# Kernel optimization log

Hardware: AMD Instinct MI355X
Metric: run time of the kernel (lower is better)

## Reference

```python
import jax, jax.numpy as jnp
import numpy as np

INPUT, HIDDEN = 2048, 128

def setup_inputs() -> dict:
    key = jax.random.key(0)
    ks = jax.random.split(key, 8)
    B, T = 64, 512
    s_ih = 1.0 / np.sqrt(HIDDEN)  # pytorch RNN init: U(-1/sqrt(H), 1/sqrt(H))
    x = jax.random.normal(ks[0], (B, T, INPUT), dtype=jnp.float32)
    W_ih = jax.random.uniform(ks[1], (HIDDEN, INPUT), jnp.float32, -s_ih, s_ih)
    W_hh = jax.random.uniform(ks[2], (HIDDEN, HIDDEN), jnp.float32, -s_ih, s_ih)
    b_ih = jax.random.uniform(ks[3], (HIDDEN,), jnp.float32, -s_ih, s_ih)
    b_hh = jax.random.uniform(ks[4], (HIDDEN,), jnp.float32, -s_ih, s_ih)
    W_fc = jax.random.uniform(ks[5], (1, HIDDEN), jnp.float32, -s_ih, s_ih)
    b_fc = jax.random.uniform(ks[6], (1,), jnp.float32, -s_ih, s_ih)
    return {"x": x, "W_ih": W_ih, "W_hh": W_hh, "b_ih": b_ih, "b_hh": b_hh,
            "W_fc": W_fc, "b_fc": b_fc}

def reference(x, W_ih, W_hh, b_ih, b_hh, W_fc, b_fc):
    B = x.shape[0]
    # Batched input projection for all timesteps: [B, T, H]
    xw = jnp.einsum('bti,hi->bth', x, W_ih) + b_ih + b_hh
    # Sequential hidden-to-hidden recurrence: h_t = tanh(xw_t + h_{t-1} @ W_hh^T)
    def step(h, xw_t):
        h_new = jnp.tanh(xw_t + h @ W_hh.T)
        return h_new, None
    h0 = jnp.zeros((B, HIDDEN), dtype=x.dtype)
    h_last, _ = jax.lax.scan(step, h0, jnp.swapaxes(xw, 0, 1))  # scan over time
    # dropout is identity in eval mode
    logits = h_last @ W_fc.T + b_fc  # [B, 1]
    return logits
```

## Files before the change

kernel.cpp:

```cpp
#include <hip/hip_runtime.h>
#include <hip/hip_bf16.h>
#include <math.h>

#define INPUT 2048
#define HIDDEN 128
#define BATCH 64
#define TSTEPS 512
#define RB 16

typedef _Float16 half_t;
typedef __attribute__((ext_vector_type(2))) _Float16 half2_t;
typedef __attribute__((ext_vector_type(8))) _Float16 f16x8;
typedef __attribute__((ext_vector_type(4))) float f32x4;

static __device__ __forceinline__ f16x8 as_f16x8(uint4 v) {
  return __builtin_bit_cast(f16x8, v);
}
static __device__ __forceinline__ unsigned int h2u(half2_t v) {
  return __builtin_bit_cast(unsigned int, v);
}
static __device__ __forceinline__ half2_t pkrtz(float a, float b) {
  return __builtin_bit_cast(half2_t, __builtin_amdgcn_cvt_pkrtz(a, b));
}
static __device__ __forceinline__ float h2f(unsigned short u) {
  return (float)__builtin_bit_cast(half_t, u);
}

static __device__ __forceinline__ float tanh_fast(float x) {
#if __has_builtin(__builtin_amdgcn_exp2f)
  const float e = __builtin_amdgcn_exp2f(x * 2.885390082f);
#else
  const float e = exp2f(x * 2.885390082f);
#endif
  return 1.f - 2.f * __builtin_amdgcn_rcpf(e + 1.f);
}

__global__ __launch_bounds__(256) void prep_kernel(
    const float* __restrict__ W_ih, const float* __restrict__ W_hh,
    uint4* __restrict__ Wg, unsigned int* __restrict__ Whh2) {
  const int id = blockIdx.x * 256 + threadIdx.x;
  const int col = id & 127;
  const int kc = id >> 7;
  const float4 a = *(const float4*)(W_ih + (size_t)col * INPUT + kc * 8);
  const float4 b = *(const float4*)(W_ih + (size_t)col * INPUT + kc * 8 + 4);
  uint4 q = {h2u(pkrtz(a.x, a.y)), h2u(pkrtz(a.z, a.w)),
             h2u(pkrtz(b.x, b.y)), h2u(pkrtz(b.z, b.w))};
  Wg[(size_t)kc * 128 + col] = q;
  if (id < 8192) {
    float2 p = ((const float2*)W_hh)[id];
    half_t ha = (half_t)p.x, hb = (half_t)p.y;
    Whh2[id] = (unsigned int)__builtin_bit_cast(unsigned short, ha) |
               ((unsigned int)__builtin_bit_cast(unsigned short, hb) << 16);
  }
}

#define GBM 64
#define GBK 64
#define GNKT (INPUT / GBK)

__global__ __launch_bounds__(256) void gemm_xw_f16(
    const float* __restrict__ x, const uint4* __restrict__ Wg,
    const float* __restrict__ b_ih, const float* __restrict__ b_hh,
    half_t* __restrict__ xw) {
  __shared__ uint4 sA[2][8][64];

  const int tid = threadIdx.x;
  const int lane = tid & 63;
  const int w = tid >> 6;
  const int wr = w >> 1, wc = w & 1;
  const int block_row = blockIdx.x * GBM;
  const int kcl = lane >> 4;
  const int l15 = lane & 15;

  const int xm = tid & 63, xkq = tid >> 6;
  const float* xsrc = x + (size_t)(block_row + xm) * INPUT + xkq * 16;

  f32x4 acc[2][4];
#pragma unroll
  for (int rt = 0; rt < 2; ++rt)
#pragma unroll
    for (int ct = 0; ct < 4; ++ct) acc[rt][ct] = (f32x4)0.f;

  float bias_c[4];
#pragma unroll
  for (int ct = 0; ct < 4; ++ct) {
    const int col = wc * 64 + ct * 16 + l15;
    bias_c[ct] = b_ih[col] + b_hh[col];
  }

  float4 xva[4], xvb[4];
  uint4 br0[8], br1[8];

  auto XLOAD = [&](int kt, float4* xv) {
    const float4* xs = (const float4*)(xsrc + kt * GBK);
#pragma unroll
    for (int j = 0; j < 4; ++j) xv[j] = xs[j];
  };
  auto XWRITE = [&](int bf, const float4* xv) {
#pragma unroll
    for (int g = 0; g < 2; ++g) {
      uint4 q = {h2u(pkrtz(xv[2 * g].x, xv[2 * g].y)),
                 h2u(pkrtz(xv[2 * g].z, xv[2 * g].w)),
                 h2u(pkrtz(xv[2 * g + 1].x, xv[2 * g + 1].y)),
                 h2u(pkrtz(xv[2 * g + 1].z, xv[2 * g + 1].w))};
      sA[bf][xkq * 2 + g][xm] = q;
    }
  };
  auto BLOAD = [&](int kt, uint4* bb) {
#pragma unroll
    for (int kf = 0; kf < 2; ++kf)
#pragma unroll
      for (int ct = 0; ct < 4; ++ct)
        bb[kf * 4 + ct] =
            Wg[(size_t)(kt * 8 + kf * 4 + kcl) * 128 + wc * 64 + ct * 16 + l15];
  };
  auto COMPUTE = [&](int bf, const uint4* bb) {
    uint4 af[2][2];
#pragma unroll
    for (int kf = 0; kf < 2; ++kf)
#pragma unroll
      for (int rt = 0; rt < 2; ++rt)
        af[kf][rt] = sA[bf][kf * 4 + kcl][wr * 32 + rt * 16 + l15];
#pragma unroll
    for (int kf = 0; kf < 2; ++kf)
#pragma unroll
      for (int rt = 0; rt < 2; ++rt)
#pragma unroll
        for (int ct = 0; ct < 4; ++ct)
          acc[rt][ct] = __builtin_amdgcn_mfma_f32_16x16x32_f16(
              as_f16x8(af[kf][rt]), as_f16x8(bb[kf * 4 + ct]), acc[rt][ct], 0, 0, 0);
  };

  XLOAD(0, xva);
  XLOAD(1, xvb);
  BLOAD(0, br0);
  XWRITE(0, xva);
  __syncthreads();

#pragma unroll 1
  for (int kt = 0; kt < GNKT; kt += 2) {
    BLOAD(kt + 1, br1);
    if (kt + 2 < GNKT) XLOAD(kt + 2, xva);
    COMPUTE(0, br0);
    XWRITE(1, xvb);
    __syncthreads();
    if (kt + 2 < GNKT) BLOAD(kt + 2, br0);
    if (kt + 3 < GNKT) XLOAD(kt + 3, xvb);
    COMPUTE(1, br1);
    if (kt + 2 < GNKT) {
      XWRITE(0, xva);
      __syncthreads();
    }
  }

  const int rbase = block_row + wr * 32 + (lane >> 4) * 4;
#pragma unroll
  for (int rt = 0; rt < 2; ++rt)
#pragma unroll
    for (int ct = 0; ct < 4; ++ct) {
      const int col = wc * 64 + ct * 16 + l15;
#pragma unroll
      for (int j = 0; j < 4; ++j) {
        const int row = rbase + rt * 16 + j;
        xw[(size_t)row * HIDDEN + col] = (half_t)(acc[rt][ct][j] + bias_c[ct]);
      }
    }
}

__global__ __launch_bounds__(256) void rnn_rec_mfma(
    const half_t* __restrict__ xw, const unsigned int* __restrict__ Whh2,
    const float* __restrict__ W_fc, const float* __restrict__ b_fc,
    float* __restrict__ out) {
  const int blk = blockIdx.x;
  const int tid = threadIdx.x;
  const int lane = tid & 63;
  const int w = tid >> 6;
  const int bl = lane & 15;
  const int g = lane >> 4;
  const int swz = (bl & 7) << 4;

  __shared__ half_t st[2][RB][HIDDEN];
  __shared__ float red[256];

  uint4 afr[2][4];
#pragma unroll
  for (int mi = 0; mi < 2; ++mi)
#pragma unroll
    for (int kt = 0; kt < 4; ++kt)
      afr[mi][kt] = *(const uint4*)(Whh2 + ((size_t)((2 * w + mi) * 16 + bl)) * 64 +
                                    kt * 16 + g * 4);

#pragma unroll
  for (int i = 0; i < 4; ++i) ((unsigned int*)st)[tid + 256 * i] = 0u;
  __syncthreads();

  const half_t* xb0 = xw + ((size_t)(blk * RB + bl) * TSTEPS) * HIDDEN + w * 32 + g * 4;
  const half_t* xb1 = xb0 + 16;

  float hh[2][4];

  auto STEP = [&](const half_t* stR, half_t* stW, ushort4 xc0, ushort4 xc1) {
    uint4 bfr[4];
#pragma unroll
    for (int kt = 0; kt < 4; ++kt) {
      const int off = (bl * 256 + kt * 64 + g * 16) ^ swz;
      bfr[kt] = *(const uint4*)((const char*)stR + off);
    }
    f32x4 a0, a1;
    a0[0] = h2f(xc0.x); a0[1] = h2f(xc0.y); a0[2] = h2f(xc0.z); a0[3] = h2f(xc0.w);
    a1[0] = h2f(xc1.x); a1[1] = h2f(xc1.y); a1[2] = h2f(xc1.z); a1[3] = h2f(xc1.w);
#pragma unroll
    for (int kt = 0; kt < 4; ++kt) {
      a0 = __builtin_amdgcn_mfma_f32_16x16x32_f16(as_f16x8(afr[0][kt]),
                                                  as_f16x8(bfr[kt]), a0, 0, 0, 0);
      a1 = __builtin_amdgcn_mfma_f32_16x16x32_f16(as_f16x8(afr[1][kt]),
                                                  as_f16x8(bfr[kt]), a1, 0, 0, 0);
    }
#pragma unroll
    for (int j = 0; j < 4; ++j) {
      hh[0][j] = tanh_fast(a0[j]);
      hh[1][j] = tanh_fast(a1[j]);
    }
    uint2 p0 = {h2u(pkrtz(hh[0][0], hh[0][1])), h2u(pkrtz(hh[0][2], hh[0][3]))};
    uint2 p1 = {h2u(pkrtz(hh[1][0], hh[1][1])), h2u(pkrtz(hh[1][2], hh[1][3]))};
    const int w0 = (bl * 256 + (2 * w + 0) * 32 + g * 8) ^ swz;
    const int w1 = (bl * 256 + (2 * w + 1) * 32 + g * 8) ^ swz;
    *(uint2*)((char*)stW + w0) = p0;
    *(uint2*)((char*)stW + w1) = p1;
    __syncthreads();
  };

  ushort4 xA0 = *(const ushort4*)(xb0);
  ushort4 xA1 = *(const ushort4*)(xb1);
  ushort4 xB0 = *(const ushort4*)(xb0 + HIDDEN);
  ushort4 xB1 = *(const ushort4*)(xb1 + HIDDEN);

  for (int t2 = 0; t2 < TSTEPS; t2 += 2) {
    ushort4 c0 = xA0, c1 = xA1;
    xA0 = *(const ushort4*)(xb0 + (size_t)(t2 + 2) * HIDDEN);
    xA1 = *(const ushort4*)(xb1 + (size_t)(t2 + 2) * HIDDEN);
    STEP(&st[0][0][0], &st[1][0][0], c0, c1);

    ushort4 d0 = xB0, d1 = xB1;
    xB0 = *(const ushort4*)(xb0 + (size_t)(t2 + 3) * HIDDEN);
    xB1 = *(const ushort4*)(xb1 + (size_t)(t2 + 3) * HIDDEN);
    STEP(&st[1][0][0], &st[0][0][0], d0, d1);
  }

  const float4 wf0 = *(const float4*)&W_fc[(2 * w + 0) * 16 + g * 4];
  const float4 wf1 = *(const float4*)&W_fc[(2 * w + 1) * 16 + g * 4];
  float partial = hh[0][0] * wf0.x + hh[0][1] * wf0.y + hh[0][2] * wf0.z +
                  hh[0][3] * wf0.w + hh[1][0] * wf1.x + hh[1][1] * wf1.y +
                  hh[1][2] * wf1.z + hh[1][3] * wf1.w;
  red[tid] = partial;
  __syncthreads();
  if (tid < RB) {
    float s = b_fc[0];
#pragma unroll
    for (int q = 0; q < 16; ++q) s += red[q * 16 + tid];
    out[blk * RB + tid] = s;
  }
}

extern "C" void kernel_launch(void* const* d_in, const int* in_sizes, int n_in,
                              void* d_out, int out_size, void* d_ws, size_t ws_size,
                              hipStream_t stream) {
  const float* x    = (const float*)d_in[0];
  const float* W_ih = (const float*)d_in[1];
  const float* W_hh = (const float*)d_in[2];
  const float* b_ih = (const float*)d_in[3];
  const float* b_hh = (const float*)d_in[4];
  const float* W_fc = (const float*)d_in[5];
  const float* b_fc = (const float*)d_in[6];

  char* ws = (char*)d_ws;
  half_t*       xwf16 = (half_t*)ws;
  uint4*        Wg    = (uint4*)(ws + (8u << 20));
  unsigned int* Whh2  = (unsigned int*)(ws + (8u << 20) + (512u << 10));

  prep_kernel<<<128, 256, 0, stream>>>(W_ih, W_hh, Wg, Whh2);
  gemm_xw_f16<<<(BATCH * TSTEPS) / GBM, 256, 0, stream>>>(x, Wg, b_ih, b_hh, xwf16);
  rnn_rec_mfma<<<BATCH / RB, 256, 0, stream>>>(xwf16, Whh2, W_fc, b_fc, (float*)d_out);
}
```

Measured before the change: 259.2 us.

## Process two 16-row batch tiles per block in the recurrence kernel

The recurrence kernel now handles 32 batch rows per block (two 16-row MFMA tiles sharing the same W_hh fragments), launching 2 blocks instead of 4. Each step issues twice as many independent MFMAs and LDS reads between barriers, so the per-step barrier and latency costs are amortised over more work. The trade-off is less parallelism across CUs and a longer dependent chain per step. The final reduction is extended to produce both tiles' outputs.

```diff
diff --git a/kernel.cpp b/kernel.cpp
--- a/kernel.cpp
+++ b/kernel.cpp
@@ -167,7 +167,7 @@
     }
 }
 
-__global__ __launch_bounds__(256) void rnn_rec_mfma(
+__global__ __launch_bounds__(256, 1) void rnn_rec_mfma2(
     const half_t* __restrict__ xw, const unsigned int* __restrict__ Whh2,
     const float* __restrict__ W_fc, const float* __restrict__ b_fc,
     float* __restrict__ out) {
@@ -176,11 +176,11 @@
   const int lane = tid & 63;
   const int w = tid >> 6;
   const int bl = lane & 15;
-  const int g = lane >> 4;
+  const int kg = lane >> 4;
   const int swz = (bl & 7) << 4;
 
-  __shared__ half_t st[2][RB][HIDDEN];
-  __shared__ float red[256];
+  __shared__ half_t st[2][2][RB][HIDDEN];
+  __shared__ float red[512];
 
   uint4 afr[2][4];
 #pragma unroll
@@ -188,77 +188,122 @@
 #pragma unroll
     for (int kt = 0; kt < 4; ++kt)
       afr[mi][kt] = *(const uint4*)(Whh2 + ((size_t)((2 * w + mi) * 16 + bl)) * 64 +
-                                    kt * 16 + g * 4);
-
-#pragma unroll
-  for (int i = 0; i < 4; ++i) ((unsigned int*)st)[tid + 256 * i] = 0u;
+                                    kt * 16 + kg * 4);
+
+#pragma unroll
+  for (int i = 0; i < 8; ++i) ((unsigned int*)st)[tid + 256 * i] = 0u;
   __syncthreads();
 
-  const half_t* xb0 = xw + ((size_t)(blk * RB + bl) * TSTEPS) * HIDDEN + w * 32 + g * 4;
-  const half_t* xb1 = xb0 + 16;
-
-  float hh[2][4];
-
-  auto STEP = [&](const half_t* stR, half_t* stW, ushort4 xc0, ushort4 xc1) {
-    uint4 bfr[4];
+  const half_t* p00 = xw + ((size_t)(blk * 32 + bl) * TSTEPS) * HIDDEN + w * 32 + kg * 4;
+  const half_t* p01 = p00 + 16;
+  const half_t* p10 = xw + ((size_t)(blk * 32 + 16 + bl) * TSTEPS) * HIDDEN + w * 32 + kg * 4;
+  const half_t* p11 = p10 + 16;
+
+  float hh[2][2][4];
+
+  int roff0[4], roff1[4];
+#pragma unroll
+  for (int kt = 0; kt < 4; ++kt) {
+    roff0[kt] = ((bl * 256 + kt * 64 + kg * 16) ^ swz);
+    roff1[kt] = roff0[kt] + 4096;
+  }
+  const int w00 = ((bl * 256 + (2 * w + 0) * 32 + kg * 8) ^ swz);
+  const int w01 = ((bl * 256 + (2 * w + 1) * 32 + kg * 8) ^ swz);
+  const int w10 = w00 + 4096, w11 = w01 + 4096;
+
+  auto STEP2 = [&](const char* stR, char* stW, ushort4 c00, ushort4 c01,
+                   ushort4 c10, ushort4 c11) {
+    uint4 b0[4], b1[4];
+#pragma unroll
+    for (int kt = 0; kt < 4; ++kt) b0[kt] = *(const uint4*)(stR + roff0[kt]);
+#pragma unroll
+    for (int kt = 0; kt < 4; ++kt) b1[kt] = *(const uint4*)(stR + roff1[kt]);
+
+    f32x4 a00, a01, a10, a11;
+    a00[0] = h2f(c00.x); a00[1] = h2f(c00.y); a00[2] = h2f(c00.z); a00[3] = h2f(c00.w);
+    a01[0] = h2f(c01.x); a01[1] = h2f(c01.y); a01[2] = h2f(c01.z); a01[3] = h2f(c01.w);
+    a10[0] = h2f(c10.x); a10[1] = h2f(c10.y); a10[2] = h2f(c10.z); a10[3] = h2f(c10.w);
+    a11[0] = h2f(c11.x); a11[1] = h2f(c11.y); a11[2] = h2f(c11.z); a11[3] = h2f(c11.w);
+
 #pragma unroll
     for (int kt = 0; kt < 4; ++kt) {
-      const int off = (bl * 256 + kt * 64 + g * 16) ^ swz;
-      bfr[kt] = *(const uint4*)((const char*)stR + off);
-    }
-    f32x4 a0, a1;
-    a0[0] = h2f(xc0.x); a0[1] = h2f(xc0.y); a0[2] = h2f(xc0.z); a0[3] = h2f(xc0.w);
-    a1[0] = h2f(xc1.x); a1[1] = h2f(xc1.y); a1[2] = h2f(xc1.z); a1[3] = h2f(xc1.w);
-#pragma unroll
-    for (int kt = 0; kt < 4; ++kt) {
-      a0 = __builtin_amdgcn_mfma_f32_16x16x32_f16(as_f16x8(afr[0][kt]),
-                                                  as_f16x8(bfr[kt]), a0, 0, 0, 0);
-      a1 = __builtin_amdgcn_mfma_f32_16x16x32_f16(as_f16x8(afr[1][kt]),
-                                                  as_f16x8(bfr[kt]), a1, 0, 0, 0);
+      a00 = __builtin_amdgcn_mfma_f32_16x16x32_f16(as_f16x8(afr[0][kt]),
+                                                   as_f16x8(b0[kt]), a00, 0, 0, 0);
+      a01 = __builtin_amdgcn_mfma_f32_16x16x32_f16(as_f16x8(afr[1][kt]),
+                                                   as_f16x8(b0[kt]), a01, 0, 0, 0);
+      a10 = __builtin_amdgcn_mfma_f32_16x16x32_f16(as_f16x8(afr[0][kt]),
+                                                   as_f16x8(b1[kt]), a10, 0, 0, 0);
+      a11 = __builtin_amdgcn_mfma_f32_16x16x32_f16(as_f16x8(afr[1][kt]),
+                                                   as_f16x8(b1[kt]), a11, 0, 0, 0);
     }
 #pragma unroll
     for (int j = 0; j < 4; ++j) {
-      hh[0][j] = tanh_fast(a0[j]);
-      hh[1][j] = tanh_fast(a1[j]);
-    }
-    uint2 p0 = {h2u(pkrtz(hh[0][0], hh[0][1])), h2u(pkrtz(hh[0][2], hh[0][3]))};
-    uint2 p1 = {h2u(pkrtz(hh[1][0], hh[1][1])), h2u(pkrtz(hh[1][2], hh[1][3]))};
-    const int w0 = (bl * 256 + (2 * w + 0) * 32 + g * 8) ^ swz;
-    const int w1 = (bl * 256 + (2 * w + 1) * 32 + g * 8) ^ swz;
-    *(uint2*)((char*)stW + w0) = p0;
-    *(uint2*)((char*)stW + w1) = p1;
+      hh[0][0][j] = tanh_fast(a00[j]);
+      hh[0][1][j] = tanh_fast(a01[j]);
+      hh[1][0][j] = tanh_fast(a10[j]);
+      hh[1][1][j] = tanh_fast(a11[j]);
+    }
+    uint2 q00 = {h2u(pkrtz(hh[0][0][0], hh[0][0][1])), h2u(pkrtz(hh[0][0][2], hh[0][0][3]))};
+    uint2 q01 = {h2u(pkrtz(hh[0][1][0], hh[0][1][1])), h2u(pkrtz(hh[0][1][2], hh[0][1][3]))};
+    uint2 q10 = {h2u(pkrtz(hh[1][0][0], hh[1][0][1])), h2u(pkrtz(hh[1][0][2], hh[1][0][3]))};
+    uint2 q11 = {h2u(pkrtz(hh[1][1][0], hh[1][1][1])), h2u(pkrtz(hh[1][1][2], hh[1][1][3]))};
+    *(uint2*)(stW + w00) = q00;
+    *(uint2*)(stW + w01) = q01;
+    *(uint2*)(stW + w10) = q10;
+    *(uint2*)(stW + w11) = q11;
     __syncthreads();
   };
 
-  ushort4 xA0 = *(const ushort4*)(xb0);
-  ushort4 xA1 = *(const ushort4*)(xb1);
-  ushort4 xB0 = *(const ushort4*)(xb0 + HIDDEN);
-  ushort4 xB1 = *(const ushort4*)(xb1 + HIDDEN);
+  char* st0 = (char*)&st[0][0][0][0];
+  char* st1 = (char*)&st[1][0][0][0];
+
+  ushort4 xa00 = *(const ushort4*)(p00);
+  ushort4 xa01 = *(const ushort4*)(p01);
+  ushort4 xa10 = *(const ushort4*)(p10);
+  ushort4 xa11 = *(const ushort4*)(p11);
+  ushort4 xb00 = *(const ushort4*)(p00 + HIDDEN);
+  ushort4 xb01 = *(const ushort4*)(p01 + HIDDEN);
+  ushort4 xb10 = *(const ushort4*)(p10 + HIDDEN);
+  ushort4 xb11 = *(const ushort4*)(p11 + HIDDEN);
 
   for (int t2 = 0; t2 < TSTEPS; t2 += 2) {
-    ushort4 c0 = xA0, c1 = xA1;
-    xA0 = *(const ushort4*)(xb0 + (size_t)(t2 + 2) * HIDDEN);
-    xA1 = *(const ushort4*)(xb1 + (size_t)(t2 + 2) * HIDDEN);
-    STEP(&st[0][0][0], &st[1][0][0], c0, c1);
-
-    ushort4 d0 = xB0, d1 = xB1;
-    xB0 = *(const ushort4*)(xb0 + (size_t)(t2 + 3) * HIDDEN);
-    xB1 = *(const ushort4*)(xb1 + (size_t)(t2 + 3) * HIDDEN);
-    STEP(&st[1][0][0], &st[0][0][0], d0, d1);
-  }
-
-  const float4 wf0 = *(const float4*)&W_fc[(2 * w + 0) * 16 + g * 4];
-  const float4 wf1 = *(const float4*)&W_fc[(2 * w + 1) * 16 + g * 4];
-  float partial = hh[0][0] * wf0.x + hh[0][1] * wf0.y + hh[0][2] * wf0.z +
-                  hh[0][3] * wf0.w + hh[1][0] * wf1.x + hh[1][1] * wf1.y +
-                  hh[1][2] * wf1.z + hh[1][3] * wf1.w;
-  red[tid] = partial;
+    const ushort4 c00 = xa00, c01 = xa01, c10 = xa10, c11 = xa11;
+    xa00 = *(const ushort4*)(p00 + (size_t)(t2 + 2) * HIDDEN);
+    xa01 = *(const ushort4*)(p01 + (size_t)(t2 + 2) * HIDDEN);
+    xa10 = *(const ushort4*)(p10 + (size_t)(t2 + 2) * HIDDEN);
+    xa11 = *(const ushort4*)(p11 + (size_t)(t2 + 2) * HIDDEN);
+    STEP2(st0, st1, c00, c01, c10, c11);
+
+    const ushort4 d00 = xb00, d01 = xb01, d10 = xb10, d11 = xb11;
+    xb00 = *(const ushort4*)(p00 + (size_t)(t2 + 3) * HIDDEN);
+    xb01 = *(const ushort4*)(p01 + (size_t)(t2 + 3) * HIDDEN);
+    xb10 = *(const ushort4*)(p10 + (size_t)(t2 + 3) * HIDDEN);
+    xb11 = *(const ushort4*)(p11 + (size_t)(t2 + 3) * HIDDEN);
+    STEP2(st1, st0, d00, d01, d10, d11);
+  }
+
+  const float4 wf0 = *(const float4*)&W_fc[(2 * w + 0) * 16 + kg * 4];
+  const float4 wf1 = *(const float4*)&W_fc[(2 * w + 1) * 16 + kg * 4];
+  float part0 = hh[0][0][0] * wf0.x + hh[0][0][1] * wf0.y + hh[0][0][2] * wf0.z +
+                hh[0][0][3] * wf0.w + hh[0][1][0] * wf1.x + hh[0][1][1] * wf1.y +
+                hh[0][1][2] * wf1.z + hh[0][1][3] * wf1.w;
+  float part1 = hh[1][0][0] * wf0.x + hh[1][0][1] * wf0.y + hh[1][0][2] * wf0.z +
+                hh[1][0][3] * wf0.w + hh[1][1][0] * wf1.x + hh[1][1][1] * wf1.y +
+                hh[1][1][2] * wf1.z + hh[1][1][3] * wf1.w;
+  red[tid] = part0;
+  red[256 + tid] = part1;
   __syncthreads();
   if (tid < RB) {
     float s = b_fc[0];
 #pragma unroll
     for (int q = 0; q < 16; ++q) s += red[q * 16 + tid];
-    out[blk * RB + tid] = s;
+    out[blk * 32 + tid] = s;
+  } else if (tid < 32) {
+    const int b2 = tid - 16;
+    float s = b_fc[0];
+#pragma unroll
+    for (int q = 0; q < 16; ++q) s += red[256 + q * 16 + b2];
+    out[blk * 32 + 16 + b2] = s;
   }
 }
 
@@ -280,5 +325,5 @@
 
   prep_kernel<<<128, 256, 0, stream>>>(W_ih, W_hh, Wg, Whh2);
   gemm_xw_f16<<<(BATCH * TSTEPS) / GBM, 256, 0, stream>>>(x, Wg, b_ih, b_hh, xwf16);
-  rnn_rec_mfma<<<BATCH / RB, 256, 0, stream>>>(xwf16, Whh2, W_fc, b_fc, (float*)d_out);
-}
+  rnn_rec_mfma2<<<2, 256, 0, stream>>>(xwf16, Whh2, W_fc, b_fc, (float*)d_out);
+}
```

Result: slower. 403.7 us (+55.7%).

## Fuse input GEMM and recurrence into one persistent kernel with per-timestep flags

Applied to the files above, without the earlier changes.

Merges the input-projection GEMM and the sequential recurrence into one launch. Four blocks run the recurrence while the rest compute xw per timestep, split-K into four slices that accumulate in order through atomic flags. The recurrence spins on each timestep's flag, so it can start before the whole GEMM finishes and overlap with it. The xw layout becomes time-major, and a large LDS pad limits blocks per CU, likely so the recurrence blocks get their own CUs. Risks are spin-wait and flag overhead, serialized split-K read-modify-writes, reduced GEMM occupancy, and reliance on the scheduler placing the recurrence blocks early.

```diff
diff --git a/kernel.cpp b/kernel.cpp
--- a/kernel.cpp
+++ b/kernel.cpp
@@ -7,6 +7,10 @@
 #define BATCH 64
 #define TSTEPS 512
 #define RB 16
+#define KSLICE 4
+#define KS (INPUT / KSLICE)
+#define GBK 64
+#define SNKT (KS / GBK)
 
 typedef _Float16 half_t;
 typedef __attribute__((ext_vector_type(2))) _Float16 half2_t;
@@ -54,133 +58,148 @@
   }
 }
 
-#define GBM 64
-#define GBK 64
-#define GNKT (INPUT / GBK)
-
-__global__ __launch_bounds__(256) void gemm_xw_f16(
+__global__ __launch_bounds__(256) void fused_kernel(
     const float* __restrict__ x, const uint4* __restrict__ Wg,
-    const float* __restrict__ b_ih, const float* __restrict__ b_hh,
-    half_t* __restrict__ xw) {
+    const unsigned int* __restrict__ Whh2, const float* __restrict__ b_ih,
+    const float* __restrict__ b_hh, const float* __restrict__ W_fc,
+    const float* __restrict__ b_fc, half_t* __restrict__ xw,
+    int* __restrict__ flags, float* __restrict__ out) {
   __shared__ uint4 sA[2][8][64];
+  __shared__ half_t st[2][RB][HIDDEN];
+  __shared__ float red[256];
+  __shared__ char lds_pad[39 * 1024];
+  if (flags == nullptr) lds_pad[threadIdx.x] = 1;
 
   const int tid = threadIdx.x;
   const int lane = tid & 63;
   const int w = tid >> 6;
-  const int wr = w >> 1, wc = w & 1;
-  const int block_row = blockIdx.x * GBM;
-  const int kcl = lane >> 4;
   const int l15 = lane & 15;
 
-  const int xm = tid & 63, xkq = tid >> 6;
-  const float* xsrc = x + (size_t)(block_row + xm) * INPUT + xkq * 16;
-
-  f32x4 acc[2][4];
-#pragma unroll
-  for (int rt = 0; rt < 2; ++rt)
-#pragma unroll
-    for (int ct = 0; ct < 4; ++ct) acc[rt][ct] = (f32x4)0.f;
-
-  float bias_c[4];
-#pragma unroll
-  for (int ct = 0; ct < 4; ++ct) {
-    const int col = wc * 64 + ct * 16 + l15;
-    bias_c[ct] = b_ih[col] + b_hh[col];
-  }
-
-  float4 xva[4], xvb[4];
-  uint4 br0[8], br1[8];
-
-  auto XLOAD = [&](int kt, float4* xv) {
-    const float4* xs = (const float4*)(xsrc + kt * GBK);
-#pragma unroll
-    for (int j = 0; j < 4; ++j) xv[j] = xs[j];
-  };
-  auto XWRITE = [&](int bf, const float4* xv) {
-#pragma unroll
-    for (int g = 0; g < 2; ++g) {
-      uint4 q = {h2u(pkrtz(xv[2 * g].x, xv[2 * g].y)),
-                 h2u(pkrtz(xv[2 * g].z, xv[2 * g].w)),
-                 h2u(pkrtz(xv[2 * g + 1].x, xv[2 * g + 1].y)),
-                 h2u(pkrtz(xv[2 * g + 1].z, xv[2 * g + 1].w))};
-      sA[bf][xkq * 2 + g][xm] = q;
-    }
-  };
-  auto BLOAD = [&](int kt, uint4* bb) {
-#pragma unroll
-    for (int kf = 0; kf < 2; ++kf)
-#pragma unroll
-      for (int ct = 0; ct < 4; ++ct)
-        bb[kf * 4 + ct] =
-            Wg[(size_t)(kt * 8 + kf * 4 + kcl) * 128 + wc * 64 + ct * 16 + l15];
-  };
-  auto COMPUTE = [&](int bf, const uint4* bb) {
-    uint4 af[2][2];
-#pragma unroll
-    for (int kf = 0; kf < 2; ++kf)
-#pragma unroll
-      for (int rt = 0; rt < 2; ++rt)
-        af[kf][rt] = sA[bf][kf * 4 + kcl][wr * 32 + rt * 16 + l15];
-#pragma unroll
-    for (int kf = 0; kf < 2; ++kf)
-#pragma unroll
-      for (int rt = 0; rt < 2; ++rt)
-#pragma unroll
-        for (int ct = 0; ct < 4; ++ct)
-          acc[rt][ct] = __builtin_amdgcn_mfma_f32_16x16x32_f16(
-              as_f16x8(af[kf][rt]), as_f16x8(bb[kf * 4 + ct]), acc[rt][ct], 0, 0, 0);
-  };
-
-  XLOAD(0, xva);
-  XLOAD(1, xvb);
-  BLOAD(0, br0);
-  XWRITE(0, xva);
-  __syncthreads();
-
-#pragma unroll 1
-  for (int kt = 0; kt < GNKT; kt += 2) {
-    BLOAD(kt + 1, br1);
-    if (kt + 2 < GNKT) XLOAD(kt + 2, xva);
-    COMPUTE(0, br0);
-    XWRITE(1, xvb);
-    __syncthreads();
-    if (kt + 2 < GNKT) BLOAD(kt + 2, br0);
-    if (kt + 3 < GNKT) XLOAD(kt + 3, xvb);
-    COMPUTE(1, br1);
-    if (kt + 2 < GNKT) {
-      XWRITE(0, xva);
-      __syncthreads();
-    }
-  }
-
-  const int rbase = block_row + wr * 32 + (lane >> 4) * 4;
-#pragma unroll
-  for (int rt = 0; rt < 2; ++rt)
+  if (blockIdx.x >= 4) {
+    const int p = blockIdx.x - 4;
+    const int t = p >> 2;
+    const int s = p & 3;
+
+    const int wr = w >> 1, wc = w & 1;
+    const int kcl = lane >> 4;
+    const int xm = tid & 63, xkq = tid >> 6;
+    const float* xsrc =
+        x + ((size_t)xm * TSTEPS + t) * INPUT + s * KS + xkq * 16;
+
+    f32x4 acc[2][4];
+#pragma unroll
+    for (int rt = 0; rt < 2; ++rt)
+#pragma unroll
+      for (int ct = 0; ct < 4; ++ct) acc[rt][ct] = (f32x4)0.f;
+
+    float bias_c[4];
 #pragma unroll
     for (int ct = 0; ct < 4; ++ct) {
       const int col = wc * 64 + ct * 16 + l15;
-#pragma unroll
-      for (int j = 0; j < 4; ++j) {
-        const int row = rbase + rt * 16 + j;
-        xw[(size_t)row * HIDDEN + col] = (half_t)(acc[rt][ct][j] + bias_c[ct]);
+      bias_c[ct] = b_ih[col] + b_hh[col];
+    }
+
+    float4 xva[4], xvb[4];
+    uint4 br0[8], br1[8];
+
+    auto XLOAD = [&](int kt, float4* xv) {
+      const float4* xs = (const float4*)(xsrc + kt * GBK);
+#pragma unroll
+      for (int j = 0; j < 4; ++j) xv[j] = xs[j];
+    };
+    auto XWRITE = [&](int bf, const float4* xv) {
+#pragma unroll
+      for (int g = 0; g < 2; ++g) {
+        uint4 q = {h2u(pkrtz(xv[2 * g].x, xv[2 * g].y)),
+                   h2u(pkrtz(xv[2 * g].z, xv[2 * g].w)),
+                   h2u(pkrtz(xv[2 * g + 1].x, xv[2 * g + 1].y)),
+                   h2u(pkrtz(xv[2 * g + 1].z, xv[2 * g + 1].w))};
+        sA[bf][xkq * 2 + g][xm] = q;
       }
-    }
-}
-
-__global__ __launch_bounds__(256) void rnn_rec_mfma(
-    const half_t* __restrict__ xw, const unsigned int* __restrict__ Whh2,
-    const float* __restrict__ W_fc, const float* __restrict__ b_fc,
-    float* __restrict__ out) {
+    };
+    auto BLOAD = [&](int kt, uint4* bb) {
+#pragma unroll
+      for (int kf = 0; kf < 2; ++kf)
+#pragma unroll
+        for (int ct = 0; ct < 4; ++ct)
+          bb[kf * 4 + ct] = Wg[(size_t)((s * SNKT + kt) * 8 + kf * 4 + kcl) * 128 +
+                               wc * 64 + ct * 16 + l15];
+    };
+    auto COMPUTE = [&](int bf, const uint4* bb) {
+      uint4 af[2][2];
+#pragma unroll
+      for (int kf = 0; kf < 2; ++kf)
+#pragma unroll
+        for (int rt = 0; rt < 2; ++rt)
+          af[kf][rt] = sA[bf][kf * 4 + kcl][wr * 32 + rt * 16 + l15];
+#pragma unroll
+      for (int kf = 0; kf < 2; ++kf)
+#pragma unroll
+        for (int rt = 0; rt < 2; ++rt)
+#pragma unroll
+          for (int ct = 0; ct < 4; ++ct)
+            acc[rt][ct] = __builtin_amdgcn_mfma_f32_16x16x32_f16(
+                as_f16x8(af[kf][rt]), as_f16x8(bb[kf * 4 + ct]), acc[rt][ct], 0, 0, 0);
+    };
+
+    XLOAD(0, xva);
+    XLOAD(1, xvb);
+    BLOAD(0, br0);
+    XWRITE(0, xva);
+    __syncthreads();
+
+#pragma unroll 1
+    for (int kt = 0; kt < SNKT; kt += 2) {
+      BLOAD(kt + 1, br1);
+      if (kt + 2 < SNKT) XLOAD(kt + 2, xva);
+      COMPUTE(0, br0);
+      XWRITE(1, xvb);
+      __syncthreads();
+      if (kt + 2 < SNKT) BLOAD(kt + 2, br0);
+      if (kt + 3 < SNKT) XLOAD(kt + 3, xvb);
+      COMPUTE(1, br1);
+      if (kt + 2 < SNKT) {
+        XWRITE(0, xva);
+        __syncthreads();
+      }
+    }
+
+    if (s != 0) {
+      if (tid == 0)
+        while (__hip_atomic_load(&flags[t], __ATOMIC_ACQUIRE,
+                                 __HIP_MEMORY_SCOPE_AGENT) != s)
+          __builtin_amdgcn_s_sleep(1);
+      __syncthreads();
+    }
+    const int rbase = wr * 32 + (lane >> 4) * 4;
+    half_t* xwt = xw + (size_t)t * (BATCH * HIDDEN);
+#pragma unroll
+    for (int rt = 0; rt < 2; ++rt)
+#pragma unroll
+      for (int ct = 0; ct < 4; ++ct) {
+        const int col = wc * 64 + ct * 16 + l15;
+#pragma unroll
+        for (int j = 0; j < 4; ++j) {
+          const int row = rbase + rt * 16 + j;
+          const size_t idx = (size_t)row * HIDDEN + col;
+          if (s == 0) {
+            xwt[idx] = (half_t)(acc[rt][ct][j] + bias_c[ct]);
+          } else {
+            xwt[idx] = (half_t)((float)xwt[idx] + acc[rt][ct][j]);
+          }
+        }
+      }
+    __syncthreads();
+    if (tid == 0)
+      __hip_atomic_store(&flags[t], s + 1, __ATOMIC_RELEASE,
+                         __HIP_MEMORY_SCOPE_AGENT);
+    return;
+  }
+
   const int blk = blockIdx.x;
-  const int tid = threadIdx.x;
-  const int lane = tid & 63;
-  const int w = tid >> 6;
   const int bl = lane & 15;
-  const int g = lane >> 4;
+  const int kg = lane >> 4;
   const int swz = (bl & 7) << 4;
-
-  __shared__ half_t st[2][RB][HIDDEN];
-  __shared__ float red[256];
 
   uint4 afr[2][4];
 #pragma unroll
@@ -188,22 +207,31 @@
 #pragma unroll
     for (int kt = 0; kt < 4; ++kt)
       afr[mi][kt] = *(const uint4*)(Whh2 + ((size_t)((2 * w + mi) * 16 + bl)) * 64 +
-                                    kt * 16 + g * 4);
+                                    kt * 16 + kg * 4);
 
 #pragma unroll
   for (int i = 0; i < 4; ++i) ((unsigned int*)st)[tid + 256 * i] = 0u;
   __syncthreads();
 
-  const half_t* xb0 = xw + ((size_t)(blk * RB + bl) * TSTEPS) * HIDDEN + w * 32 + g * 4;
+  const half_t* xb0 = xw + (size_t)(blk * RB + bl) * HIDDEN + w * 32 + kg * 4;
   const half_t* xb1 = xb0 + 16;
+#define TSTR ((size_t)(BATCH * HIDDEN))
 
   float hh[2][4];
+
+  auto aload = [&](int tt) {
+    return __hip_atomic_load(&flags[tt], __ATOMIC_ACQUIRE,
+                             __HIP_MEMORY_SCOPE_AGENT);
+  };
+  auto waitf = [&](int tt) {
+    while (aload(tt) != KSLICE) __builtin_amdgcn_s_sleep(2);
+  };
 
   auto STEP = [&](const half_t* stR, half_t* stW, ushort4 xc0, ushort4 xc1) {
     uint4 bfr[4];
 #pragma unroll
     for (int kt = 0; kt < 4; ++kt) {
-      const int off = (bl * 256 + kt * 64 + g * 16) ^ swz;
+      const int off = (bl * 256 + kt * 64 + kg * 16) ^ swz;
       bfr[kt] = *(const uint4*)((const char*)stR + off);
     }
     f32x4 a0, a1;
@@ -223,42 +251,51 @@
     }
     uint2 p0 = {h2u(pkrtz(hh[0][0], hh[0][1])), h2u(pkrtz(hh[0][2], hh[0][3]))};
     uint2 p1 = {h2u(pkrtz(hh[1][0], hh[1][1])), h2u(pkrtz(hh[1][2], hh[1][3]))};
-    const int w0 = (bl * 256 + (2 * w + 0) * 32 + g * 8) ^ swz;
-    const int w1 = (bl * 256 + (2 * w + 1) * 32 + g * 8) ^ swz;
+    const int w0 = (bl * 256 + (2 * w + 0) * 32 + kg * 8) ^ swz;
+    const int w1 = (bl * 256 + (2 * w + 1) * 32 + kg * 8) ^ swz;
     *(uint2*)((char*)stW + w0) = p0;
     *(uint2*)((char*)stW + w1) = p1;
     __syncthreads();
   };
 
+  waitf(0);
   ushort4 xA0 = *(const ushort4*)(xb0);
   ushort4 xA1 = *(const ushort4*)(xb1);
-  ushort4 xB0 = *(const ushort4*)(xb0 + HIDDEN);
-  ushort4 xB1 = *(const ushort4*)(xb1 + HIDDEN);
+  waitf(1);
+  ushort4 xB0 = *(const ushort4*)(xb0 + TSTR);
+  ushort4 xB1 = *(const ushort4*)(xb1 + TSTR);
 
   for (int t2 = 0; t2 < TSTEPS; t2 += 2) {
-    ushort4 c0 = xA0, c1 = xA1;
-    xA0 = *(const ushort4*)(xb0 + (size_t)(t2 + 2) * HIDDEN);
-    xA1 = *(const ushort4*)(xb1 + (size_t)(t2 + 2) * HIDDEN);
+    const ushort4 c0 = xA0, c1 = xA1;
+    int f2 = (t2 + 2 < TSTEPS) ? aload(t2 + 2) : KSLICE;
     STEP(&st[0][0][0], &st[1][0][0], c0, c1);
-
-    ushort4 d0 = xB0, d1 = xB1;
-    xB0 = *(const ushort4*)(xb0 + (size_t)(t2 + 3) * HIDDEN);
-    xB1 = *(const ushort4*)(xb1 + (size_t)(t2 + 3) * HIDDEN);
+    if (t2 + 2 < TSTEPS) {
+      while (f2 != KSLICE) { __builtin_amdgcn_s_sleep(1); f2 = aload(t2 + 2); }
+      xA0 = *(const ushort4*)(xb0 + (size_t)(t2 + 2) * TSTR);
+      xA1 = *(const ushort4*)(xb1 + (size_t)(t2 + 2) * TSTR);
+    }
+    const ushort4 d0 = xB0, d1 = xB1;
+    int f3 = (t2 + 3 < TSTEPS) ? aload(t2 + 3) : KSLICE;
     STEP(&st[1][0][0], &st[0][0][0], d0, d1);
+    if (t2 + 3 < TSTEPS) {
+      while (f3 != KSLICE) { __builtin_amdgcn_s_sleep(1); f3 = aload(t2 + 3); }
+      xB0 = *(const ushort4*)(xb0 + (size_t)(t2 + 3) * TSTR);
+      xB1 = *(const ushort4*)(xb1 + (size_t)(t2 + 3) * TSTR);
+    }
   }
 
-  const float4 wf0 = *(const float4*)&W_fc[(2 * w + 0) * 16 + g * 4];
-  const float4 wf1 = *(const float4*)&W_fc[(2 * w + 1) * 16 + g * 4];
+  const float4 wf0 = *(const float4*)&W_fc[(2 * w + 0) * 16 + kg * 4];
+  const float4 wf1 = *(const float4*)&W_fc[(2 * w + 1) * 16 + kg * 4];
   float partial = hh[0][0] * wf0.x + hh[0][1] * wf0.y + hh[0][2] * wf0.z +
                   hh[0][3] * wf0.w + hh[1][0] * wf1.x + hh[1][1] * wf1.y +
                   hh[1][2] * wf1.z + hh[1][3] * wf1.w;
   red[tid] = partial;
   __syncthreads();
   if (tid < RB) {
-    float s = b_fc[0];
-#pragma unroll
-    for (int q = 0; q < 16; ++q) s += red[q * 16 + tid];
-    out[blk * RB + tid] = s;
+    float ssum = b_fc[0];
+#pragma unroll
+    for (int q = 0; q < 16; ++q) ssum += red[q * 16 + tid];
+    out[blk * RB + tid] = ssum;
   }
 }
 
@@ -274,11 +311,13 @@
   const float* b_fc = (const float*)d_in[6];
 
   char* ws = (char*)d_ws;
-  half_t*       xwf16 = (half_t*)ws;
-  uint4*        Wg    = (uint4*)(ws + (8u << 20));
-  unsigned int* Whh2  = (unsigned int*)(ws + (8u << 20) + (512u << 10));
-
+  int*          flags = (int*)ws;
+  half_t*       xwf16 = (half_t*)(ws + 4096);
+  uint4*        Wg    = (uint4*)(ws + 4096 + (8u << 20));
+  unsigned int* Whh2  = (unsigned int*)(ws + 4096 + (8u << 20) + (512u << 10));
+
+  hipMemsetAsync(ws, 0, 4096, stream);
   prep_kernel<<<128, 256, 0, stream>>>(W_ih, W_hh, Wg, Whh2);
-  gemm_xw_f16<<<(BATCH * TSTEPS) / GBM, 256, 0, stream>>>(x, Wg, b_ih, b_hh, xwf16);
-  rnn_rec_mfma<<<BATCH / RB, 256, 0, stream>>>(xwf16, Whh2, W_fc, b_fc, (float*)d_out);
-}
+  fused_kernel<<<4 + TSTEPS * KSLICE, 256, 0, stream>>>(
+      x, Wg, Whh2, b_ih, b_hh, W_fc, b_fc, xwf16, flags, (float*)d_out);
+}
```

Result: slower. 747.7 us (+188.4%).
